# Performance work log

Measured on AMD Instinct MI355X. Metric: run time of the kernel, lower is better.

Reference implementation:

```python
import jax, jax.numpy as jnp
import numpy as np

B = 131072      # batch of states
STATE = 32      # state dim
HIDDEN = 256    # MLP hidden width
NOUT = 32       # MLP outputs (summed after relu -> scalar value)
ACT = 8         # action dim (QP size)
QP_ITERS = 30   # BoxCDQP coordinate-descent sweeps


def setup_inputs() -> dict:
    key = jax.random.key(0)
    ks = jax.random.split(key, 8)
    sc = lambda fan: 1.0 / np.sqrt(fan)
    x = jax.random.normal(ks[0], (B, STATE), jnp.float32)
    t = jnp.zeros((1,), jnp.float32)
    W0 = jax.random.normal(ks[1], (STATE, HIDDEN), jnp.float32) * sc(STATE)
    b0 = jnp.zeros((HIDDEN,), jnp.float32)
    W1 = jax.random.normal(ks[2], (HIDDEN, HIDDEN), jnp.float32) * sc(HIDDEN)
    b1 = jnp.zeros((HIDDEN,), jnp.float32)
    W2 = jax.random.normal(ks[3], (HIDDEN, HIDDEN), jnp.float32) * sc(HIDDEN)
    b2 = jnp.zeros((HIDDEN,), jnp.float32)
    Wout = jax.random.normal(ks[4], (HIDDEN, NOUT), jnp.float32) * sc(HIDDEN)
    bout = jnp.zeros((NOUT,), jnp.float32)
    G = jax.random.normal(ks[5], (STATE, ACT), jnp.float32) * sc(STATE)
    A = jax.random.normal(ks[6], (ACT, ACT), jnp.float32)
    R = A @ A.T / ACT + jnp.eye(ACT, dtype=jnp.float32)  # symmetric PD cost
    lower = -jnp.ones((ACT,), jnp.float32)
    upper = jnp.ones((ACT,), jnp.float32)
    return dict(x=x, t=t, W0=W0, b0=b0, W1=W1, b1=b1, W2=W2, b2=b2,
                Wout=Wout, bout=bout, G=G, R=R, lower=lower, upper=upper)


def _v(xi, W0, b0, W1, b1, W2, b2, Wout, bout):
    # v(x) = sum(relu(MLP(angle_rep(x)))), angle_rep = identity here
    h = jax.nn.softplus(xi @ W0 + b0)
    h = jax.nn.softplus(h @ W1 + b1)
    h = jax.nn.softplus(h @ W2 + b2)
    return jnp.sum(jax.nn.relu(h @ Wout + bout))


def _box_cdqp(Q, c, lo, hi):
    # BoxCDQP: min 0.5 u^T Q u + c^T u  s.t. lo <= u <= hi, cyclic coord descent
    diag = jnp.diag(Q)

    def sweep(u, _):
        for i in range(ACT):  # ACT is small and static -> unrolled
            gi = Q[i] @ u + c[i]
            u = u.at[i].set(jnp.clip(u[i] - gi / diag[i], lo[i], hi[i]))
        return u, None

    u, _ = jax.lax.scan(sweep, jnp.zeros_like(c), None, length=QP_ITERS)
    return u


def reference(x, t, W0, b0, W1, b1, W2, b2, Wout, bout, G, R, lower, upper):
    # dv/dx per sample via grad of scalar v, batched with vmap
    dvdx = jax.vmap(
        lambda xi: jax.grad(_v)(xi, W0, b0, W1, b1, W2, b2, Wout, bout)
    )(x)                                  # [B, STATE]
    c = dvdx @ G                          # [B, ACT] linear QP term (dvdx @ gx)
    Q = 2.0 * R                           # params_obj = (2*R, dvdx_gx)
    u = jax.vmap(lambda ci: _box_cdqp(Q, ci, lower, upper))(c)  # [B, ACT]
    return u
```

## Files before the change

### kernel.cpp

```cpp
#include <hip/hip_runtime.h>
#include <math.h>

typedef float f4 __attribute__((ext_vector_type(4)));
typedef float f2 __attribute__((ext_vector_type(2)));

#define THREADS 256
#define HID 256
#define SMP 16

__global__ void k_prep(const float* __restrict__ W1, const float* __restrict__ W2,
                       const float* __restrict__ Wout, float* __restrict__ ws) {
  float* W1T = ws;
  float* W2T = ws + 65536;
  float* WoutT = ws + 131072;
  int tid = blockIdx.x * 256 + threadIdx.x;
  if (tid < 65536) {
    int k = tid >> 8, n = tid & 255;
    W1T[tid] = W1[n * 256 + k];
    W2T[tid] = W2[n * 256 + k];
    if (tid < 8192) {
      int k2 = tid >> 8, n2 = tid & 255;
      WoutT[tid] = Wout[n2 * 32 + k2];
    }
  }
}

__device__ __forceinline__ float sp_cr(float z) {
  float az = fabsf(z);
  float e  = (float)exp(-(double)az);
  float lp = (float)log1p((double)e);
  return fmaxf(z, 0.0f) + lp;
}

__device__ __forceinline__ float sig_from_h(float h) {
  return 1.0f - __expf(-h);
}


template <int SEL>
__device__ __forceinline__ f2 pk_mul_b(f2 h, f2 w) {
  f2 d;
  if constexpr (SEL == 0)
    asm("v_pk_mul_f32 %0, %1, %2 op_sel:[0,0] op_sel_hi:[0,1]"
        : "=v"(d) : "v"(h), "v"(w));
  else
    asm("v_pk_mul_f32 %0, %1, %2 op_sel:[1,0] op_sel_hi:[1,1]"
        : "=v"(d) : "v"(h), "v"(w));
  return d;
}

__device__ __forceinline__ f2 pk_add(f2 a, f2 b) {
  f2 d;
  asm("v_pk_add_f32 %0, %1, %2" : "=v"(d) : "v"(a), "v"(b));
  return d;
}

template <int SEL>
__device__ __forceinline__ void pk_fma_b(f2& a, f2 h, f2 w) {
  if constexpr (SEL == 0)
    asm("v_pk_fma_f32 %0, %1, %2, %0 op_sel:[0,0,0] op_sel_hi:[0,1,1]"
        : "+v"(a) : "v"(h), "v"(w));
  else
    asm("v_pk_fma_f32 %0, %1, %2, %0 op_sel:[1,0,0] op_sel_hi:[1,1,1]"
        : "+v"(a) : "v"(h), "v"(w));
}

template <bool FWD, int SEL>
__device__ __forceinline__ void mac4(f2 (&a)[2], f2 hp, f4 wq) {
  f2 w01 = __builtin_shufflevector(wq, wq, 0, 1);
  f2 w23 = __builtin_shufflevector(wq, wq, 2, 3);
  if constexpr (FWD) {
    a[0] = pk_add(a[0], pk_mul_b<SEL>(hp, w01));
    a[1] = pk_add(a[1], pk_mul_b<SEL>(hp, w23));
  } else {
    pk_fma_b<SEL>(a[0], hp, w01);
    pk_fma_b<SEL>(a[1], hp, w23);
  }
}

#define GLOAD4(r0, r1, r2, r3, ptr)                                      \
  asm volatile("global_load_dwordx4 %0, %4, off\n\t"                     \
               "global_load_dwordx4 %1, %4, off offset:1024\n\t"         \
               "global_load_dwordx4 %2, %4, off offset:2048\n\t"         \
               "global_load_dwordx4 %3, %4, off offset:3072"             \
               : "=v"(r0), "=v"(r1), "=v"(r2), "=v"(r3)                  \
               : "v"(ptr))

#define WAIT4(r0, r1, r2, r3)                                            \
  asm volatile("s_waitcnt vmcnt(4)"                                      \
               : "+v"(r0), "+v"(r1), "+v"(r2), "+v"(r3))

#define WAIT0(r0, r1, r2, r3)                                            \
  asm volatile("s_waitcnt vmcnt(0)"                                      \
               : "+v"(r0), "+v"(r1), "+v"(r2), "+v"(r3))

template <int K, bool FWD>
__device__ __forceinline__ void mac_group(f2 (&acc)[4][2],
                                          const float* __restrict__ hin,
                                          int sA, int g, const f4& w0,
                                          const f4& w1, const f4& w2,
                                          const f4& w3) {
  #pragma unroll
  for (int s = 0; s < 4; ++s) {
    f4 hq = *(const f4*)&hin[(size_t)(sA + s) * K + g * 4];
    f2 h01 = __builtin_shufflevector(hq, hq, 0, 1);
    f2 h23 = __builtin_shufflevector(hq, hq, 2, 3);
    mac4<FWD, 0>(acc[s], h01, w0);
    mac4<FWD, 1>(acc[s], h01, w1);
    mac4<FWD, 0>(acc[s], h23, w2);
    mac4<FWD, 1>(acc[s], h23, w3);
  }
}

template <int K, bool FWD>
__device__ __forceinline__ void layer_g(const float* __restrict__ Wbase,
                                        const float* __restrict__ hin,
                                        int sA, int l, f2 (&acc)[4][2]) {
  #pragma unroll
  for (int s = 0; s < 4; ++s) {
    acc[s][0] = (f2){0.f, 0.f};
    acc[s][1] = (f2){0.f, 0.f};
  }
  const float* wp = Wbase + l * 4;
  constexpr int NG = K / 4;
  f4 a0, a1, a2, a3, b0, b1, b2, b3;
  GLOAD4(a0, a1, a2, a3, wp);
  GLOAD4(b0, b1, b2, b3, wp + 1024);
  #pragma unroll 1
  for (int g = 0; g <= NG - 4; g += 2) {
    WAIT4(a0, a1, a2, a3);
    mac_group<K, FWD>(acc, hin, sA, g, a0, a1, a2, a3);
    GLOAD4(a0, a1, a2, a3, wp + (size_t)(g + 2) * 1024);
    WAIT4(b0, b1, b2, b3);
    mac_group<K, FWD>(acc, hin, sA, g + 1, b0, b1, b2, b3);
    GLOAD4(b0, b1, b2, b3, wp + (size_t)(g + 3) * 1024);
  }
  WAIT4(a0, a1, a2, a3);
  mac_group<K, FWD>(acc, hin, sA, NG - 2, a0, a1, a2, a3);
  WAIT0(b0, b1, b2, b3);
  mac_group<K, FWD>(acc, hin, sA, NG - 1, b0, b1, b2, b3);
}

__device__ __forceinline__ void sp_store(const f2 (&a)[2],
                                         const float* __restrict__ b,
                                         float* __restrict__ dstrow, int l) {
  f4 bv = *(const f4*)&b[l * 4];
  f4 o;
  o[0] = sp_cr(a[0][0] + bv[0]);
  o[1] = sp_cr(a[0][1] + bv[1]);
  o[2] = sp_cr(a[1][0] + bv[2]);
  o[3] = sp_cr(a[1][1] + bv[3]);
  *(f4*)&dstrow[l * 4] = o;
}

__device__ __forceinline__ void sig_store(const f2 (&a)[2],
                                          float* __restrict__ hrow, int l) {
  f4 h = *(f4*)&hrow[l * 4];
  f4 d;
  d[0] = a[0][0] * sig_from_h(h[0]);
  d[1] = a[0][1] * sig_from_h(h[1]);
  d[2] = a[1][0] * sig_from_h(h[2]);
  d[3] = a[1][1] * sig_from_h(h[3]);
  *(f4*)&hrow[l * 4] = d;
}

__global__ __launch_bounds__(THREADS, 3) void k_main(
    const float* __restrict__ x,
    const float* __restrict__ W0, const float* __restrict__ b0,
    const float* __restrict__ W1, const float* __restrict__ b1,
    const float* __restrict__ W2, const float* __restrict__ b2,
    const float* __restrict__ Wout, const float* __restrict__ bout,
    const float* __restrict__ G, const float* __restrict__ ws,
    float* __restrict__ out) {
  __shared__ float xs[SMP][32];
  __shared__ float ha[SMP][HID];
  __shared__ float hb[SMP][HID];
  __shared__ float hc[SMP][HID];
  __shared__ float zm[SMP][32];

  const float* W1T = ws;
  const float* W2T = ws + 65536;
  const float* WoutT = ws + 131072;

  const int tid = threadIdx.x;
  const int w = tid >> 6;
  const int l = tid & 63;
  const int sA = w * 4;
  const int s0 = blockIdx.x * SMP;

  for (int i = tid; i < SMP * 32; i += THREADS) {
    xs[i >> 5][i & 31] = x[(size_t)s0 * 32 + i];
  }
  __syncthreads();

  f2 acc[4][2];

  layer_g<32, true>(W0, &xs[0][0], sA, l, acc);
  sp_store(acc[0], b0, &ha[sA + 0][0], l);
  sp_store(acc[1], b0, &ha[sA + 1][0], l);
  sp_store(acc[2], b0, &ha[sA + 2][0], l);
  sp_store(acc[3], b0, &ha[sA + 3][0], l);

  layer_g<256, true>(W1, &ha[0][0], sA, l, acc);
  sp_store(acc[0], b1, &hb[sA + 0][0], l);
  sp_store(acc[1], b1, &hb[sA + 1][0], l);
  sp_store(acc[2], b1, &hb[sA + 2][0], l);
  sp_store(acc[3], b1, &hb[sA + 3][0], l);

  layer_g<256, true>(W2, &hb[0][0], sA, l, acc);
  sp_store(acc[0], b2, &hc[sA + 0][0], l);
  sp_store(acc[1], b2, &hc[sA + 1][0], l);
  sp_store(acc[2], b2, &hc[sA + 2][0], l);
  sp_store(acc[3], b2, &hc[sA + 3][0], l);
  __syncthreads();

  {
#pragma clang fp contract(off)
    #pragma unroll
    for (int rep = 0; rep < 2; ++rep) {
      int idx = tid + rep * THREADS;
      int s = idx >> 5, j = idx & 31;
      const float* wrow = WoutT + (size_t)j * 256;
      float acc0 = 0.0f;
      #pragma unroll 4
      for (int k = 0; k < 256; k += 4) {
        f4 hv = *(const f4*)&hc[s][k];
        f4 wv = *(const f4*)&wrow[k];
        #pragma unroll
        for (int kk = 0; kk < 4; ++kk) {
          float p = hv[kk] * wv[kk];
          acc0 = acc0 + p;
        }
      }
      zm[s][j] = (acc0 + bout[j] > 0.0f) ? 1.0f : 0.0f;
    }
  }
  __syncthreads();

  layer_g<32, false>(WoutT, &zm[0][0], sA, l, acc);
  sig_store(acc[0], &hc[sA + 0][0], l);
  sig_store(acc[1], &hc[sA + 1][0], l);
  sig_store(acc[2], &hc[sA + 2][0], l);
  sig_store(acc[3], &hc[sA + 3][0], l);

  layer_g<256, false>(W2T, &hc[0][0], sA, l, acc);
  sig_store(acc[0], &hb[sA + 0][0], l);
  sig_store(acc[1], &hb[sA + 1][0], l);
  sig_store(acc[2], &hb[sA + 2][0], l);
  sig_store(acc[3], &hb[sA + 3][0], l);

  layer_g<256, false>(W1T, &hb[0][0], sA, l, acc);
  sig_store(acc[0], &ha[sA + 0][0], l);
  sig_store(acc[1], &ha[sA + 1][0], l);
  sig_store(acc[2], &ha[sA + 2][0], l);
  sig_store(acc[3], &ha[sA + 3][0], l);
  __syncthreads();

  {
    #pragma unroll
    for (int rep = 0; rep < 2; ++rep) {
      int idx = tid + rep * THREADS;
      int s = idx >> 5, j = idx & 31;
      const float* wrow = W0 + (size_t)j * 256;
      float acc0 = 0.0f;
      #pragma unroll 4
      for (int k = 0; k < 256; k += 4) {
        f4 hv = *(const f4*)&ha[s][k];
        f4 wv = *(const f4*)&wrow[k];
        #pragma unroll
        for (int kk = 0; kk < 4; ++kk) {
          acc0 = fmaf(hv[kk], wv[kk], acc0);
        }
      }
      zm[s][j] = acc0;
    }
  }
  __syncthreads();

  if (tid < SMP * 8) {
    int s = tid >> 3, a = tid & 7;
    float acc0 = 0.0f;
    #pragma unroll
    for (int j = 0; j < 32; ++j) acc0 = fmaf(zm[s][j], G[j * 8 + a], acc0);
    out[(size_t)(s0 + s) * 8 + a] = acc0;
  }
}

__global__ __launch_bounds__(256) void k_qp(float* __restrict__ out,
                                            const float* __restrict__ R,
                                            const float* __restrict__ lower,
                                            const float* __restrict__ upper) {
  int t = blockIdx.x * 256 + threadIdx.x;
  float q[8][8], u[8], cc[8], lo[8], hi[8], dg[8];
  #pragma unroll
  for (int i = 0; i < 8; ++i) {
    lo[i] = lower[i];
    hi[i] = upper[i];
    u[i] = 0.0f;
    cc[i] = out[(size_t)t * 8 + i];
    #pragma unroll
    for (int j = 0; j < 8; ++j) q[i][j] = 2.0f * R[i * 8 + j];
  }
  #pragma unroll
  for (int i = 0; i < 8; ++i) dg[i] = q[i][i];

  #pragma unroll 1
  for (int it = 0; it < 30; ++it) {
    #pragma unroll
    for (int i = 0; i < 8; ++i) {
      float g = cc[i];
      #pragma unroll
      for (int j = 0; j < 8; ++j) g = fmaf(q[i][j], u[j], g);
      float v = u[i] - g / dg[i];
      u[i] = fminf(fmaxf(v, lo[i]), hi[i]);
    }
  }
  #pragma unroll
  for (int i = 0; i < 8; ++i) out[(size_t)t * 8 + i] = u[i];
}

extern "C" void kernel_launch(void* const* d_in, const int* in_sizes, int n_in,
                              void* d_out, int out_size, void* d_ws, size_t ws_size,
                              hipStream_t stream) {
  const float* x    = (const float*)d_in[0];
  const float* W0   = (const float*)d_in[2];
  const float* b0   = (const float*)d_in[3];
  const float* W1   = (const float*)d_in[4];
  const float* b1   = (const float*)d_in[5];
  const float* W2   = (const float*)d_in[6];
  const float* b2   = (const float*)d_in[7];
  const float* Wout = (const float*)d_in[8];
  const float* bout = (const float*)d_in[9];
  const float* G    = (const float*)d_in[10];
  const float* R    = (const float*)d_in[11];
  const float* lower= (const float*)d_in[12];
  const float* upper= (const float*)d_in[13];
  float* out = (float*)d_out;
  float* ws  = (float*)d_ws;

  const int B = in_sizes[0] / 32;

  k_prep<<<256, 256, 0, stream>>>(W1, W2, Wout, ws);
  k_main<<<B / SMP, THREADS, 0, stream>>>(x, W0, b0, W1, b1, W2, b2,
                                          Wout, bout, G, ws, out);
  k_qp<<<B / 256, 256, 0, stream>>>(out, R, lower, upper);
}
```

Before: 2.056 ms.

## Use single-wave blocks processing eight samples each to double weight reuse

Each block becomes one 64-thread wave that handles 8 samples. Previously a 256-thread block split 16 samples into 4 per wave. Every weight vector fetched from global memory is now applied to twice as many samples, halving weight traffic per sample. Because the block is a single wave, all __syncthreads barriers are removed and the input tile is loaded with one vectorised load per thread. The cost is twice as many accumulator registers and a lower launch-bounds occupancy hint, which may reduce latency hiding.

```diff
diff --git a/kernel.cpp b/kernel.cpp
--- a/kernel.cpp
+++ b/kernel.cpp
@@ -4,9 +4,9 @@
 typedef float f4 __attribute__((ext_vector_type(4)));
 typedef float f2 __attribute__((ext_vector_type(2)));
 
-#define THREADS 256
+#define THREADS 64
 #define HID 256
-#define SMP 16
+#define SMP 8
 
 __global__ void k_prep(const float* __restrict__ W1, const float* __restrict__ W2,
                        const float* __restrict__ Wout, float* __restrict__ ws) {
@@ -95,14 +95,13 @@
                : "+v"(r0), "+v"(r1), "+v"(r2), "+v"(r3))
 
 template <int K, bool FWD>
-__device__ __forceinline__ void mac_group(f2 (&acc)[4][2],
+__device__ __forceinline__ void mac_group(f2 (&acc)[SMP][2],
                                           const float* __restrict__ hin,
-                                          int sA, int g, const f4& w0,
-                                          const f4& w1, const f4& w2,
-                                          const f4& w3) {
-  #pragma unroll
-  for (int s = 0; s < 4; ++s) {
-    f4 hq = *(const f4*)&hin[(size_t)(sA + s) * K + g * 4];
+                                          int g, const f4& w0, const f4& w1,
+                                          const f4& w2, const f4& w3) {
+  #pragma unroll
+  for (int s = 0; s < SMP; ++s) {
+    f4 hq = *(const f4*)&hin[(size_t)s * K + g * 4];
     f2 h01 = __builtin_shufflevector(hq, hq, 0, 1);
     f2 h23 = __builtin_shufflevector(hq, hq, 2, 3);
     mac4<FWD, 0>(acc[s], h01, w0);
@@ -115,9 +114,9 @@
 template <int K, bool FWD>
 __device__ __forceinline__ void layer_g(const float* __restrict__ Wbase,
                                         const float* __restrict__ hin,
-                                        int sA, int l, f2 (&acc)[4][2]) {
-  #pragma unroll
-  for (int s = 0; s < 4; ++s) {
+                                        int l, f2 (&acc)[SMP][2]) {
+  #pragma unroll
+  for (int s = 0; s < SMP; ++s) {
     acc[s][0] = (f2){0.f, 0.f};
     acc[s][1] = (f2){0.f, 0.f};
   }
@@ -129,16 +128,16 @@
   #pragma unroll 1
   for (int g = 0; g <= NG - 4; g += 2) {
     WAIT4(a0, a1, a2, a3);
-    mac_group<K, FWD>(acc, hin, sA, g, a0, a1, a2, a3);
+    mac_group<K, FWD>(acc, hin, g, a0, a1, a2, a3);
     GLOAD4(a0, a1, a2, a3, wp + (size_t)(g + 2) * 1024);
     WAIT4(b0, b1, b2, b3);
-    mac_group<K, FWD>(acc, hin, sA, g + 1, b0, b1, b2, b3);
+    mac_group<K, FWD>(acc, hin, g + 1, b0, b1, b2, b3);
     GLOAD4(b0, b1, b2, b3, wp + (size_t)(g + 3) * 1024);
   }
   WAIT4(a0, a1, a2, a3);
-  mac_group<K, FWD>(acc, hin, sA, NG - 2, a0, a1, a2, a3);
+  mac_group<K, FWD>(acc, hin, NG - 2, a0, a1, a2, a3);
   WAIT0(b0, b1, b2, b3);
-  mac_group<K, FWD>(acc, hin, sA, NG - 1, b0, b1, b2, b3);
+  mac_group<K, FWD>(acc, hin, NG - 1, b0, b1, b2, b3);
 }
 
 __device__ __forceinline__ void sp_store(const f2 (&a)[2],
@@ -164,7 +163,7 @@
   *(f4*)&hrow[l * 4] = d;
 }
 
-__global__ __launch_bounds__(THREADS, 3) void k_main(
+__global__ __launch_bounds__(THREADS, 2) void k_main(
     const float* __restrict__ x,
     const float* __restrict__ W0, const float* __restrict__ b0,
     const float* __restrict__ W1, const float* __restrict__ b1,
@@ -183,41 +182,32 @@
   const float* WoutT = ws + 131072;
 
   const int tid = threadIdx.x;
-  const int w = tid >> 6;
-  const int l = tid & 63;
-  const int sA = w * 4;
+  const int l = tid;
   const int s0 = blockIdx.x * SMP;
 
-  for (int i = tid; i < SMP * 32; i += THREADS) {
-    xs[i >> 5][i & 31] = x[(size_t)s0 * 32 + i];
-  }
-  __syncthreads();
-
-  f2 acc[4][2];
-
-  layer_g<32, true>(W0, &xs[0][0], sA, l, acc);
-  sp_store(acc[0], b0, &ha[sA + 0][0], l);
-  sp_store(acc[1], b0, &ha[sA + 1][0], l);
-  sp_store(acc[2], b0, &ha[sA + 2][0], l);
-  sp_store(acc[3], b0, &ha[sA + 3][0], l);
-
-  layer_g<256, true>(W1, &ha[0][0], sA, l, acc);
-  sp_store(acc[0], b1, &hb[sA + 0][0], l);
-  sp_store(acc[1], b1, &hb[sA + 1][0], l);
-  sp_store(acc[2], b1, &hb[sA + 2][0], l);
-  sp_store(acc[3], b1, &hb[sA + 3][0], l);
-
-  layer_g<256, true>(W2, &hb[0][0], sA, l, acc);
-  sp_store(acc[0], b2, &hc[sA + 0][0], l);
-  sp_store(acc[1], b2, &hc[sA + 1][0], l);
-  sp_store(acc[2], b2, &hc[sA + 2][0], l);
-  sp_store(acc[3], b2, &hc[sA + 3][0], l);
-  __syncthreads();
+  {
+    const f4* xsrc = (const f4*)(x + (size_t)s0 * 32);
+    ((f4*)xs)[tid] = xsrc[tid];
+  }
+
+  f2 acc[SMP][2];
+
+  layer_g<32, true>(W0, &xs[0][0], l, acc);
+  #pragma unroll
+  for (int s = 0; s < SMP; ++s) sp_store(acc[s], b0, &ha[s][0], l);
+
+  layer_g<256, true>(W1, &ha[0][0], l, acc);
+  #pragma unroll
+  for (int s = 0; s < SMP; ++s) sp_store(acc[s], b1, &hb[s][0], l);
+
+  layer_g<256, true>(W2, &hb[0][0], l, acc);
+  #pragma unroll
+  for (int s = 0; s < SMP; ++s) sp_store(acc[s], b2, &hc[s][0], l);
 
   {
 #pragma clang fp contract(off)
     #pragma unroll
-    for (int rep = 0; rep < 2; ++rep) {
+    for (int rep = 0; rep < 4; ++rep) {
       int idx = tid + rep * THREADS;
       int s = idx >> 5, j = idx & 31;
       const float* wrow = WoutT + (size_t)j * 256;
@@ -235,30 +225,22 @@
       zm[s][j] = (acc0 + bout[j] > 0.0f) ? 1.0f : 0.0f;
     }
   }
-  __syncthreads();
-
-  layer_g<32, false>(WoutT, &zm[0][0], sA, l, acc);
-  sig_store(acc[0], &hc[sA + 0][0], l);
-  sig_store(acc[1], &hc[sA + 1][0], l);
-  sig_store(acc[2], &hc[sA + 2][0], l);
-  sig_store(acc[3], &hc[sA + 3][0], l);
-
-  layer_g<256, false>(W2T, &hc[0][0], sA, l, acc);
-  sig_store(acc[0], &hb[sA + 0][0], l);
-  sig_store(acc[1], &hb[sA + 1][0], l);
-  sig_store(acc[2], &hb[sA + 2][0], l);
-  sig_store(acc[3], &hb[sA + 3][0], l);
-
-  layer_g<256, false>(W1T, &hb[0][0], sA, l, acc);
-  sig_store(acc[0], &ha[sA + 0][0], l);
-  sig_store(acc[1], &ha[sA + 1][0], l);
-  sig_store(acc[2], &ha[sA + 2][0], l);
-  sig_store(acc[3], &ha[sA + 3][0], l);
-  __syncthreads();
+
+  layer_g<32, false>(WoutT, &zm[0][0], l, acc);
+  #pragma unroll
+  for (int s = 0; s < SMP; ++s) sig_store(acc[s], &hc[s][0], l);
+
+  layer_g<256, false>(W2T, &hc[0][0], l, acc);
+  #pragma unroll
+  for (int s = 0; s < SMP; ++s) sig_store(acc[s], &hb[s][0], l);
+
+  layer_g<256, false>(W1T, &hb[0][0], l, acc);
+  #pragma unroll
+  for (int s = 0; s < SMP; ++s) sig_store(acc[s], &ha[s][0], l);
 
   {
     #pragma unroll
-    for (int rep = 0; rep < 2; ++rep) {
+    for (int rep = 0; rep < 4; ++rep) {
       int idx = tid + rep * THREADS;
       int s = idx >> 5, j = idx & 31;
       const float* wrow = W0 + (size_t)j * 256;
@@ -275,9 +257,8 @@
       zm[s][j] = acc0;
     }
   }
-  __syncthreads();
-
-  if (tid < SMP * 8) {
+
+  {
     int s = tid >> 3, a = tid & 7;
     float acc0 = 0.0f;
     #pragma unroll
```

Result: slower. 2.170 ms (+5.5%).
